# Kernel tuning notes

Measured on AMD Instinct MI355X. Metric: run time of the kernel, lower is better.

Reference implementation:

```python
import jax, jax.numpy as jnp
import numpy as np

K = 16  # number of piecewise-linear intervals (fixed in params_set)


def setup_inputs() -> dict:
    key = jax.random.key(0)
    k1, k2 = jax.random.split(key)
    B, S, D = 4, 4096, 2048
    x = jax.random.normal(k1, (B, S, D), dtype=jnp.float32)
    threshold = jnp.ones((1,), dtype=jnp.float32)          # alpha > 0
    theta = 0.1 * jax.random.normal(k2, (K,), dtype=jnp.float32)
    dst = jnp.arange(K, dtype=jnp.float32) / K             # delta * arange(K), delta = 1/K
    return {
        "x": x,
        "threshold": threshold,
        "theta": theta,
        "dst": dst,
        "Qn": 0,
        "Qp": 15,                 # 2**4 - 1 (activation, num_bits=4)
        "num_elements": B * S * D,
    }


def reference(x, threshold, theta, dst, Qn, Qp, num_elements):
    # LCQ_quantizer.forward (non 2-bit-weight path) -> LCQ_fast_core.forward
    s = float(Qp)
    theta_tmp = jax.nn.softmax(theta)                       # softmax over dim 0
    gamma = theta_tmp * K                                   # theta_tmp / delta
    beta = jnp.concatenate(
        [jnp.zeros((1,), theta_tmp.dtype), jnp.cumsum(theta_tmp)[: K - 1]]
    )
    alpha = threshold                                       # shape (1,), broadcasts

    flag_middle = (jnp.abs(x) < alpha).astype(x.dtype)
    flag_high = 1.0 - flag_middle
    x_tmp = jnp.abs(x) / alpha

    # compress: searchsorted bin lookup + piecewise affine
    idx = jnp.searchsorted(dst, x_tmp, side="right")        # in [1, K]
    y = gamma[idx - 1] * (x_tmp - dst[idx - 1]) + beta[idx - 1]
    y_q = jnp.round(y * s) / s                              # uniform round-quantize

    # expand: second searchsorted + inverse affine
    idx_q = jnp.searchsorted(beta, y_q, side="right")       # in [1, K]
    z_mid = (y_q - beta[idx_q - 1]) / gamma[idx_q - 1] + dst[idx_q - 1]

    z = jnp.sign(x) * alpha * (z_mid * flag_middle + flag_high)
    return z
```

## Files before the change

### kernel.cpp

```cpp
#include <hip/hip_runtime.h>
#include <math.h>

#define KB 16

typedef float vf4 __attribute__((ext_vector_type(4)));

__device__ __forceinline__ float lcq_core(float xv, float alpha, float rcp_alpha,
                                          const float2* __restrict__ s_gb,
                                          const float* __restrict__ s_zval)
{
    float a   = fabsf(xv);
    float xt  = __fmul_rn(a, rcp_alpha);
    float t16 = __fmul_rn(xt, 16.0f);
    float jf  = fminf(t16, 15.0f);
    int   j   = (int)jf;
    float2 gb = s_gb[j];
    float dj  = __fmul_rn(floorf(jf), 0.0625f);
    float y   = __fadd_rn(__fmul_rn(gb.x, __fsub_rn(xt, dj)), gb.y);
    float t   = rintf(__fmul_rn(y, 15.0f));
    int   m   = (int)fminf(t, 15.0f);
    float v   = (a < alpha) ? s_zval[m] : 1.0f;
    float r   = __fmul_rn(alpha, v);
    return copysignf(r, xv);
}

__global__ __launch_bounds__(256) void lcq_kernel(
    const float* __restrict__ x,
    const float* __restrict__ thr,
    const float* __restrict__ theta,
    float* __restrict__ out,
    long long n)
{
    __shared__ float2 s_gb[KB];
    __shared__ float  s_zval[KB];
    __shared__ float  s_scal[2];

    if (threadIdx.x == 0) {
        float th[KB];
        float mx = theta[0];
        th[0] = mx;
        #pragma unroll
        for (int i = 1; i < KB; ++i) { th[i] = theta[i]; mx = fmaxf(mx, th[i]); }
        float ex[KB];
        float sum = 0.0f;
        #pragma unroll
        for (int i = 0; i < KB; ++i) { ex[i] = expf(__fsub_rn(th[i], mx)); sum = __fadd_rn(sum, ex[i]); }
        float sm[KB];
        #pragma unroll
        for (int i = 0; i < KB; ++i) sm[i] = __fdiv_rn(ex[i], sum);

        float beta[KB], gamma[KB];
        beta[0] = 0.0f;
        float c = sm[0];
        #pragma unroll
        for (int i = 1; i < KB; ++i) { beta[i] = c; c = __fadd_rn(c, sm[i]); }
        #pragma unroll
        for (int i = 0; i < KB; ++i) gamma[i] = __fmul_rn(sm[i], 16.0f);

        #pragma unroll
        for (int i = 0; i < KB; ++i) s_gb[i] = make_float2(gamma[i], beta[i]);

        for (int m = 0; m < KB; ++m) {
            float yq = __fdiv_rn((float)m, 15.0f);
            int iq = 0;
            #pragma unroll
            for (int i = 1; i < KB; ++i) iq += (beta[i] <= yq) ? 1 : 0;
            s_zval[m] = __fadd_rn(__fdiv_rn(__fsub_rn(yq, beta[iq]), gamma[iq]),
                                  (float)iq * 0.0625f);
        }
        float alpha = thr[0];
        s_scal[0] = alpha;
        s_scal[1] = __fdiv_rn(1.0f, alpha);
    }
    __syncthreads();

    const float alpha = s_scal[0];
    const float rcpa  = s_scal[1];

    const long long n4ll = n >> 2;
    const vf4* __restrict__ x4 = (const vf4*)x;
    vf4* __restrict__ o4 = (vf4*)out;

    const unsigned base = blockIdx.x * 1024u + threadIdx.x;

    if ((long long)(blockIdx.x + 1) * 1024ll <= n4ll) {
        vf4 v0 = __builtin_nontemporal_load(&x4[base]);
        vf4 v1 = __builtin_nontemporal_load(&x4[base + 256u]);
        vf4 v2 = __builtin_nontemporal_load(&x4[base + 512u]);
        vf4 v3 = __builtin_nontemporal_load(&x4[base + 768u]);
        vf4 r0, r1, r2, r3;
        r0.x = lcq_core(v0.x, alpha, rcpa, s_gb, s_zval);
        r0.y = lcq_core(v0.y, alpha, rcpa, s_gb, s_zval);
        r0.z = lcq_core(v0.z, alpha, rcpa, s_gb, s_zval);
        r0.w = lcq_core(v0.w, alpha, rcpa, s_gb, s_zval);
        r1.x = lcq_core(v1.x, alpha, rcpa, s_gb, s_zval);
        r1.y = lcq_core(v1.y, alpha, rcpa, s_gb, s_zval);
        r1.z = lcq_core(v1.z, alpha, rcpa, s_gb, s_zval);
        r1.w = lcq_core(v1.w, alpha, rcpa, s_gb, s_zval);
        r2.x = lcq_core(v2.x, alpha, rcpa, s_gb, s_zval);
        r2.y = lcq_core(v2.y, alpha, rcpa, s_gb, s_zval);
        r2.z = lcq_core(v2.z, alpha, rcpa, s_gb, s_zval);
        r2.w = lcq_core(v2.w, alpha, rcpa, s_gb, s_zval);
        r3.x = lcq_core(v3.x, alpha, rcpa, s_gb, s_zval);
        r3.y = lcq_core(v3.y, alpha, rcpa, s_gb, s_zval);
        r3.z = lcq_core(v3.z, alpha, rcpa, s_gb, s_zval);
        r3.w = lcq_core(v3.w, alpha, rcpa, s_gb, s_zval);
        __builtin_nontemporal_store(r0, &o4[base]);
        __builtin_nontemporal_store(r1, &o4[base + 256u]);
        __builtin_nontemporal_store(r2, &o4[base + 512u]);
        __builtin_nontemporal_store(r3, &o4[base + 768u]);
    } else {
        #pragma unroll
        for (int k = 0; k < 4; ++k) {
            long long i = (long long)base + k * 256;
            if (i < n4ll) {
                vf4 v = x4[i];
                vf4 r;
                r.x = lcq_core(v.x, alpha, rcpa, s_gb, s_zval);
                r.y = lcq_core(v.y, alpha, rcpa, s_gb, s_zval);
                r.z = lcq_core(v.z, alpha, rcpa, s_gb, s_zval);
                r.w = lcq_core(v.w, alpha, rcpa, s_gb, s_zval);
                o4[i] = r;
            }
        }
        if (blockIdx.x == gridDim.x - 1) {
            for (long long k = (n4ll << 2) + threadIdx.x; k < n; k += 256) {
                out[k] = lcq_core(x[k], alpha, rcpa, s_gb, s_zval);
            }
        }
    }
}

extern "C" void kernel_launch(void* const* d_in, const int* in_sizes, int n_in,
                              void* d_out, int out_size, void* d_ws, size_t ws_size,
                              hipStream_t stream) {
    const float* x     = (const float*)d_in[0];
    const float* thr   = (const float*)d_in[1];
    const float* theta = (const float*)d_in[2];
    float* out = (float*)d_out;

    long long n = (long long)in_sizes[0];
    long long n4 = n >> 2;
    long long grid = (n4 + 1023) / 1024;
    if (grid < 1) grid = 1;
    dim3 block(256);
    hipLaunchKernelGGL(lcq_kernel, dim3((unsigned)grid), block, 0, stream,
                       x, thr, theta, out, n);
}
```

Measured before the change: 236.1 us.

## Precompute quantizer lookup tables in a separate setup kernel

Moves the per-block softmax, cumulative-sum and inverse-table computation, previously done serially by thread 0 of every block, into a single-thread setup kernel that writes a 50-float table to workspace. The main kernel now has threads cooperatively load that table into shared memory before processing. This removes a redundant serial prologue from each of the thousands of blocks. The cost is a second kernel launch plus a global read of the table per block.

```diff
diff --git a/kernel.cpp b/kernel.cpp
--- a/kernel.cpp
+++ b/kernel.cpp
@@ -4,6 +4,54 @@
 #define KB 16
 
 typedef float vf4 __attribute__((ext_vector_type(4)));
+
+#define WS_FLOATS 50
+
+__global__ __launch_bounds__(64) void lcq_setup_kernel(
+    const float* __restrict__ thr,
+    const float* __restrict__ theta,
+    float* __restrict__ ws)
+{
+    if (threadIdx.x != 0) return;
+
+    float th[KB];
+    float mx = theta[0];
+    th[0] = mx;
+    #pragma unroll
+    for (int i = 1; i < KB; ++i) { th[i] = theta[i]; mx = fmaxf(mx, th[i]); }
+    float ex[KB];
+    float sum = 0.0f;
+    #pragma unroll
+    for (int i = 0; i < KB; ++i) { ex[i] = expf(__fsub_rn(th[i], mx)); sum = __fadd_rn(sum, ex[i]); }
+    float sm[KB];
+    #pragma unroll
+    for (int i = 0; i < KB; ++i) sm[i] = __fdiv_rn(ex[i], sum);
+
+    float beta[KB], gamma[KB];
+    beta[0] = 0.0f;
+    float c = sm[0];
+    #pragma unroll
+    for (int i = 1; i < KB; ++i) { beta[i] = c; c = __fadd_rn(c, sm[i]); }
+    #pragma unroll
+    for (int i = 0; i < KB; ++i) gamma[i] = __fmul_rn(sm[i], 16.0f);
+
+    #pragma unroll
+    for (int i = 0; i < KB; ++i) {
+        ws[2 * i]     = gamma[i];
+        ws[2 * i + 1] = beta[i];
+    }
+    for (int m = 0; m < KB; ++m) {
+        float yq = __fdiv_rn((float)m, 15.0f);
+        int iq = 0;
+        #pragma unroll
+        for (int i = 1; i < KB; ++i) iq += (beta[i] <= yq) ? 1 : 0;
+        ws[32 + m] = __fadd_rn(__fdiv_rn(__fsub_rn(yq, beta[iq]), gamma[iq]),
+                               (float)iq * 0.0625f);
+    }
+    float alpha = thr[0];
+    ws[48] = alpha;
+    ws[49] = __fdiv_rn(1.0f, alpha);
+}
 
 __device__ __forceinline__ float lcq_core(float xv, float alpha, float rcp_alpha,
                                           const float2* __restrict__ s_gb,
@@ -26,56 +74,19 @@
 
 __global__ __launch_bounds__(256) void lcq_kernel(
     const float* __restrict__ x,
-    const float* __restrict__ thr,
-    const float* __restrict__ theta,
+    const float* __restrict__ ws,
     float* __restrict__ out,
     long long n)
 {
-    __shared__ float2 s_gb[KB];
-    __shared__ float  s_zval[KB];
-    __shared__ float  s_scal[2];
+    __shared__ __align__(16) float s_tab[WS_FLOATS];
 
-    if (threadIdx.x == 0) {
-        float th[KB];
-        float mx = theta[0];
-        th[0] = mx;
-        #pragma unroll
-        for (int i = 1; i < KB; ++i) { th[i] = theta[i]; mx = fmaxf(mx, th[i]); }
-        float ex[KB];
-        float sum = 0.0f;
-        #pragma unroll
-        for (int i = 0; i < KB; ++i) { ex[i] = expf(__fsub_rn(th[i], mx)); sum = __fadd_rn(sum, ex[i]); }
-        float sm[KB];
-        #pragma unroll
-        for (int i = 0; i < KB; ++i) sm[i] = __fdiv_rn(ex[i], sum);
-
-        float beta[KB], gamma[KB];
-        beta[0] = 0.0f;
-        float c = sm[0];
-        #pragma unroll
-        for (int i = 1; i < KB; ++i) { beta[i] = c; c = __fadd_rn(c, sm[i]); }
-        #pragma unroll
-        for (int i = 0; i < KB; ++i) gamma[i] = __fmul_rn(sm[i], 16.0f);
-
-        #pragma unroll
-        for (int i = 0; i < KB; ++i) s_gb[i] = make_float2(gamma[i], beta[i]);
-
-        for (int m = 0; m < KB; ++m) {
-            float yq = __fdiv_rn((float)m, 15.0f);
-            int iq = 0;
-            #pragma unroll
-            for (int i = 1; i < KB; ++i) iq += (beta[i] <= yq) ? 1 : 0;
-            s_zval[m] = __fadd_rn(__fdiv_rn(__fsub_rn(yq, beta[iq]), gamma[iq]),
-                                  (float)iq * 0.0625f);
-        }
-        float alpha = thr[0];
-        s_scal[0] = alpha;
-        s_scal[1] = __fdiv_rn(1.0f, alpha);
-    }
+    if (threadIdx.x < WS_FLOATS) s_tab[threadIdx.x] = ws[threadIdx.x];
     __syncthreads();
 
-    const float alpha = s_scal[0];
-    const float rcpa  = s_scal[1];
+    const float2* s_gb   = (const float2*)s_tab;
+    const float*  s_zval = s_tab + 32;
+    const float alpha = s_tab[48];
+    const float rcpa  = s_tab[49];
 
     const long long n4ll = n >> 2;
     const vf4* __restrict__ x4 = (const vf4*)x;
@@ -138,12 +149,15 @@
     const float* thr   = (const float*)d_in[1];
     const float* theta = (const float*)d_in[2];
     float* out = (float*)d_out;
+    float* ws  = (float*)d_ws;
 
     long long n = (long long)in_sizes[0];
     long long n4 = n >> 2;
     long long grid = (n4 + 1023) / 1024;
     if (grid < 1) grid = 1;
-    dim3 block(256);
-    hipLaunchKernelGGL(lcq_kernel, dim3((unsigned)grid), block, 0, stream,
-                       x, thr, theta, out, n);
+
+    hipLaunchKernelGGL(lcq_setup_kernel, dim3(1), dim3(64), 0, stream,
+                       thr, theta, ws);
+    hipLaunchKernelGGL(lcq_kernel, dim3((unsigned)grid), dim3(256), 0, stream,
+                       x, ws, out, n);
 }
```

After: 238.9 us. About the same (+1.2%).
